# Optimization experiments

Measured on AMD Instinct MI355X. Metric: run time of the kernel, lower is better.

## Reference

```python
import jax, jax.numpy as jnp
import numpy as np

ITERATIONS = 10
EPS = 1e-8
ALPHA = 1.0
BETA = 1.0


def _conv3x3x3(x):
    # all-ones 3x3x3 kernel, padding=1 (SAME), single channel; NCDHW layout
    k = jnp.ones((1, 1, 3, 3, 3), x.dtype)
    return jax.lax.conv_general_dilated(
        x, k, window_strides=(1, 1, 1), padding='SAME',
        dimension_numbers=('NCDHW', 'OIDHW', 'NCDHW'))


def _soft_skeletonize(x):
    x = jax.nn.sigmoid(x)
    skeleton = x
    for _ in range(ITERATIONS):
        eroded = (_conv3x3x3(skeleton) > 0).astype(x.dtype)
        opened = (_conv3x3x3(eroded) > 0).astype(x.dtype)
        skeleton = jnp.clip(skeleton - opened, 0.0, 1.0)
    return skeleton


def _count_components(binary):
    neighbors = _conv3x3x3(binary)
    mask = binary > 0
    cnt = jnp.sum(mask).astype(binary.dtype)
    # torch.mean(neighbors[mask] + eps) == sum((neighbors+eps)*mask)/cnt
    mean_nb = jnp.sum(jnp.where(mask, neighbors + EPS, 0.0)) / jnp.maximum(cnt, 1.0)
    return (cnt / mean_nb)[None]


def setup_inputs() -> dict:
    key = jax.random.key(0)
    k1, k2 = jax.random.split(key)
    pred = jax.random.normal(k1, (2, 1, 192, 192, 192), dtype=jnp.float32)
    target = jax.random.uniform(k2, (2, 1, 192, 192, 192), dtype=jnp.float32)
    return {"pred": pred, "target": target}


def reference(pred, target):
    pred_prob = jax.nn.sigmoid(pred)
    # NOTE: module applies sigmoid again inside _soft_skeletonize (faithful)
    pred_skeleton = _soft_skeletonize(pred_prob)
    target_skeleton = _soft_skeletonize(target)

    intersection = jnp.sum(pred_skeleton * target_skeleton)
    union = jnp.sum(pred_skeleton) + jnp.sum(target_skeleton)
    skeleton_loss = 1.0 - (2.0 * intersection + EPS) / (union + EPS)

    pred_binary = (pred_prob > 0.5).astype(pred.dtype)
    target_binary = target  # .float() no-op
    pred_components = _count_components(pred_binary)
    target_components = _count_components(target_binary)
    connectivity_loss = jnp.mean(jnp.abs(pred_components - target_components))

    return ALPHA * skeleton_loss + BETA * connectivity_loss
```

## Files before the change

### kernel.cpp

```cpp
#include <hip/hip_runtime.h>
#include <math.h>

#define NN 192
#define PLANE (NN * NN)
#define VOL (NN * NN * NN)
#define ZCHUNK 12
#define RP 96
#define NBIN 8
#define EPSF 1e-8f

template <int MODE>
__device__ __forceinline__ float bval(float u) {
  return (MODE == 0) ? ((u > 0.f) ? 1.f : 0.f) : u;
}

struct PlaneR {
  float4 a, b, c, d;
};

__device__ __forceinline__ void loadP(const float* __restrict__ base, int z,
                                      int offA, int offB, int offC, int offD,
                                      int xoff, PlaneR& P) {
  const int zz = min(max(z, 0), NN - 1);
  const float* p = base + (size_t)zz * PLANE;
  P.a = *(const float4*)(p + offA + xoff);
  P.b = *(const float4*)(p + offB + xoff);
  P.c = *(const float4*)(p + offC + xoff);
  P.d = *(const float4*)(p + offD + xoff);
}

template <int MODE>
__device__ __forceinline__ void consume2(const PlaneR& P, float mA, float mD, float mz,
                                         int lane, float4& sY, float4& sZ,
                                         float4& cY, float4& cZ) {
  const float a0 = bval<MODE>(P.a.x), a1 = bval<MODE>(P.a.y), a2 = bval<MODE>(P.a.z), a3 = bval<MODE>(P.a.w);
  const float b0 = bval<MODE>(P.b.x), b1 = bval<MODE>(P.b.y), b2 = bval<MODE>(P.b.z), b3 = bval<MODE>(P.b.w);
  const float c0 = bval<MODE>(P.c.x), c1 = bval<MODE>(P.c.y), c2 = bval<MODE>(P.c.z), c3 = bval<MODE>(P.c.w);
  const float d0 = bval<MODE>(P.d.x), d1 = bval<MODE>(P.d.y), d2 = bval<MODE>(P.d.z), d3 = bval<MODE>(P.d.w);
  const float u0 = b0 + c0, u1 = b1 + c1, u2 = b2 + c2, u3 = b3 + c3;
  const float tY0 = fmaf(a0, mA, u0), tY1 = fmaf(a1, mA, u1), tY2 = fmaf(a2, mA, u2), tY3 = fmaf(a3, mA, u3);
  const float tZ0 = fmaf(d0, mD, u0), tZ1 = fmaf(d1, mD, u1), tZ2 = fmaf(d2, mD, u2), tZ3 = fmaf(d3, mD, u3);
  const float upY = __shfl_up(tY3, 1), dnY = __shfl_down(tY0, 1);
  const float upZ = __shfl_up(tZ3, 1), dnZ = __shfl_down(tZ0, 1);
  const float tlY = (lane == 0) ? 0.f : upY;
  const float trY = (lane >= 47) ? 0.f : dnY;
  const float tlZ = (lane == 0) ? 0.f : upZ;
  const float trZ = (lane >= 47) ? 0.f : dnZ;
  const float pY01 = tY0 + tY1, pY23 = tY2 + tY3;
  const float pZ01 = tZ0 + tZ1, pZ23 = tZ2 + tZ3;
  sY.x = (tlY + pY01) * mz; sY.y = (pY01 + tY2) * mz; sY.z = (tY1 + pY23) * mz; sY.w = (pY23 + trY) * mz;
  sZ.x = (tlZ + pZ01) * mz; sZ.y = (pZ01 + tZ2) * mz; sZ.z = (tZ1 + pZ23) * mz; sZ.w = (pZ23 + trZ) * mz;
  cY.x = b0; cY.y = b1; cY.z = b2; cY.w = b3;
  cZ.x = c0; cZ.y = c1; cZ.z = c2; cZ.w = c3;
}

#define ACC1(C, SP, SC, SN)                                   \
  {                                                           \
    float m = ((C) > 0.f) ? act : 0.f;                        \
    cnt += m;                                                 \
    acc = fmaf(m, ((SP) + (SC)) + (SN), acc);                 \
  }

#define ACCUM8(snY, snZ)                      \
  ACC1(cY.x, spY.x, scY.x, (snY).x)           \
  ACC1(cY.y, spY.y, scY.y, (snY).y)           \
  ACC1(cY.z, spY.z, scY.z, (snY).z)           \
  ACC1(cY.w, spY.w, scY.w, (snY).w)           \
  ACC1(cZ.x, spZ.x, scZ.x, (snZ).x)           \
  ACC1(cZ.y, spZ.y, scZ.y, (snZ).y)           \
  ACC1(cZ.z, spZ.z, scZ.z, (snZ).z)           \
  ACC1(cZ.w, spZ.w, scZ.w, (snZ).w)

#define ROTATE(snY, snZ, cnY, cnZ) \
  spY = scY; scY = snY; spZ = scZ; scZ = snZ; cY = cnY; cZ = cnZ;

#define STEP_R(PSLOT, I)                                                   \
  {                                                                        \
    float4 snY, snZ, cnY, cnZ;                                             \
    consume2<MODE>(PSLOT, mA, mD, 1.f, lane, snY, snZ, cnY, cnZ);          \
    loadP(base, z0 + 4 + (I), offA, offB, offC, offD, xoff, PSLOT);        \
    ACCUM8(snY, snZ);                                                      \
    ROTATE(snY, snZ, cnY, cnZ);                                            \
  }

#define STEP_E(PSLOT, MZ)                                                  \
  {                                                                        \
    float4 snY, snZ, cnY, cnZ;                                             \
    consume2<MODE>(PSLOT, mA, mD, (MZ), lane, snY, snZ, cnY, cnZ);         \
    ACCUM8(snY, snZ);                                                      \
    ROTATE(snY, snZ, cnY, cnZ);                                            \
  }

template <int MODE>
__device__ __forceinline__ void unit2(const float* __restrict__ base, int y0, int z0,
                                      int xoff, float act, int lane,
                                      float& cnt, float& acc) {
  const int offB = y0 * NN;
  const int offA = (y0 > 0 ? y0 - 1 : 0) * NN;
  const int offC = (y0 + 1) * NN;
  const int offD = (y0 + 2 < NN ? y0 + 2 : NN - 1) * NN;
  const float mA = (y0 > 0) ? 1.f : 0.f;
  const float mD = (y0 + 2 < NN) ? 1.f : 0.f;
  const float mzLo = (z0 > 0) ? 1.f : 0.f;
  const float mzHi = (z0 + ZCHUNK < NN) ? 1.f : 0.f;

  PlaneR P0, P1, P2;
  loadP(base, z0 - 1, offA, offB, offC, offD, xoff, P0);
  loadP(base, z0,     offA, offB, offC, offD, xoff, P1);
  loadP(base, z0 + 1, offA, offB, offC, offD, xoff, P2);

  float4 spY, scY, spZ, scZ, cY, cZ, j1, j2;
  consume2<MODE>(P0, mA, mD, mzLo, lane, spY, spZ, j1, j2);
  loadP(base, z0 + 2, offA, offB, offC, offD, xoff, P0);
  consume2<MODE>(P1, mA, mD, 1.f, lane, scY, scZ, cY, cZ);
  loadP(base, z0 + 3, offA, offB, offC, offD, xoff, P1);

#pragma unroll 1
  for (int i = 0; i < 9; i += 3) {
    STEP_R(P2, i + 0);
    STEP_R(P0, i + 1);
    STEP_R(P1, i + 2);
  }
  STEP_E(P2, 1.f);
  STEP_E(P0, 1.f);
  STEP_E(P1, mzHi);
}

__global__ void init_ws(float* __restrict__ ws) {
  if (threadIdx.x < NBIN * 16) ws[threadIdx.x] = 0.f;
}

__global__ __launch_bounds__(64, 4) void skel_main(const float* __restrict__ pred,
                                                   const float* __restrict__ target,
                                                   float* __restrict__ ws) {
  const int b = blockIdx.x;
  const int vol = b & 3;
  const int r = b >> 2;
  const int zc = r / RP;
  const int yp = r % RP;
  const int z0 = zc * ZCHUNK;
  const int y0 = 2 * yp;
  const float* base = (vol < 2 ? pred : target) + (size_t)(vol & 1) * VOL;

  const int lane = threadIdx.x;
  const int xoff = 4 * min(lane, 47);
  const float act = (lane < 48) ? 1.f : 0.f;

  float cnt = 0.f, acc = 0.f;
  if (vol < 2) unit2<0>(base, y0, z0, xoff, act, lane, cnt, acc);
  else         unit2<1>(base, y0, z0, xoff, act, lane, cnt, acc);

#pragma unroll
  for (int o = 32; o > 0; o >>= 1) {
    cnt += __shfl_down(cnt, o);
    acc += __shfl_down(acc, o);
  }
  if (lane == 0) {
    const int off = (vol < 2) ? 0 : 2;
    float* slot = &ws[((r & (NBIN - 1)) << 4) + off];
    atomicAdd(slot + 0, cnt);
    atomicAdd(slot + 1, acc);
  }
}

__global__ void finalize(const float* __restrict__ ws, float* __restrict__ out) {
  if (threadIdx.x == 0 && blockIdx.x == 0) {
    float cp = 0.f, ap = 0.f, ct = 0.f, at = 0.f;
#pragma unroll
    for (int i = 0; i < NBIN; ++i) {
      cp += ws[i * 16 + 0];
      ap += ws[i * 16 + 1];
      ct += ws[i * 16 + 2];
      at += ws[i * 16 + 3];
    }
    float mp = (ap + EPSF * cp) / fmaxf(cp, 1.f);
    float Pc = cp / mp;
    float mt = (at + EPSF * ct) / fmaxf(ct, 1.f);
    float Tc = ct / mt;
    out[0] = fabsf(Pc - Tc);
  }
}

extern "C" void kernel_launch(void* const* d_in, const int* in_sizes, int n_in,
                              void* d_out, int out_size, void* d_ws, size_t ws_size,
                              hipStream_t stream) {
  const float* pred = (const float*)d_in[0];
  const float* target = (const float*)d_in[1];
  float* ws = (float*)d_ws;
  float* out = (float*)d_out;

  init_ws<<<1, 128, 0, stream>>>(ws);
  skel_main<<<dim3(6144), dim3(64), 0, stream>>>(pred, target, ws);
  finalize<<<1, 64, 0, stream>>>(ws, out);
}
```

Measured before the change: 163.2 us.

## Stage 10-row y-slabs through LDS ring buffer with 256-thread blocks

Replaces per-wave direct global loads of 4 rows per z-plane with a 4-slot LDS ring buffer. A 256-thread block cooperatively loads a 10-row slab (8 rows plus halos) per plane, and each of its 4 waves reads its own 4-row window from LDS. This cuts redundant global reads of the y-halo rows, from about 2x down to about 1.25x, and lengthens the z-chunk to 24, which lowers z-halo overhead. Block indexing is remapped so the low bits select the z-chunk, presumably to spread work across XCDs. The cost is a __syncthreads per plane, fewer and larger blocks (768), and an extra block-level reduction through shared memory.

```diff
diff --git a/kernel.cpp b/kernel.cpp
--- a/kernel.cpp
+++ b/kernel.cpp
@@ -3,9 +3,11 @@
 
 #define NN 192
 #define PLANE (NN * NN)
-#define VOL (NN * NN * NN)
-#define ZCHUNK 12
-#define RP 96
+#define VOLSZ (NN * NN * NN)
+#define ZC 24
+#define SLABR 8
+#define NSLAB (NN / SLABR)
+#define SLOTF (10 * NN)
 #define NBIN 8
 #define EPSF 1e-8f
 
@@ -17,17 +19,6 @@
 struct PlaneR {
   float4 a, b, c, d;
 };
-
-__device__ __forceinline__ void loadP(const float* __restrict__ base, int z,
-                                      int offA, int offB, int offC, int offD,
-                                      int xoff, PlaneR& P) {
-  const int zz = min(max(z, 0), NN - 1);
-  const float* p = base + (size_t)zz * PLANE;
-  P.a = *(const float4*)(p + offA + xoff);
-  P.b = *(const float4*)(p + offB + xoff);
-  P.c = *(const float4*)(p + offC + xoff);
-  P.d = *(const float4*)(p + offD + xoff);
-}
 
 template <int MODE>
 __device__ __forceinline__ void consume2(const PlaneR& P, float mA, float mD, float mz,
@@ -71,95 +62,141 @@
   ACC1(cZ.z, spZ.z, scZ.z, (snZ).z)           \
   ACC1(cZ.w, spZ.w, scZ.w, (snZ).w)
 
-#define ROTATE(snY, snZ, cnY, cnZ) \
-  spY = scY; scY = snY; spZ = scZ; scZ = snZ; cY = cnY; cZ = cnZ;
-
-#define STEP_R(PSLOT, I)                                                   \
+__device__ __forceinline__ void ldsReadP(const float* pl, int slotF, int rbaseF, int xoff, PlaneR& P) {
+  const float* p = pl + slotF + rbaseF;
+  P.a = *(const float4*)(p + 0 * NN + xoff);
+  P.b = *(const float4*)(p + 1 * NN + xoff);
+  P.c = *(const float4*)(p + 2 * NN + xoff);
+  P.d = *(const float4*)(p + 3 * NN + xoff);
+}
+
+__device__ __forceinline__ void stageIssue(const float* __restrict__ base, int z, int gRow0,
+                                           int tid, int nQ, float4& g0, float4& g1) {
+  const int zz = min(max(z, 0), NN - 1);
+  const float* gp = base + (size_t)zz * PLANE + gRow0 * NN;
+  g0 = *(const float4*)(gp + 4 * tid);
+  if (tid + 256 < nQ) g1 = *(const float4*)(gp + 4 * (tid + 256));
+}
+
+__device__ __forceinline__ void stageWrite(float* pl, int slotF, int shiftF, int tid, int nQ,
+                                           const float4& g0, const float4& g1) {
+  float* q = pl + slotF + shiftF;
+  *(float4*)(q + 4 * tid) = g0;
+  if (tid + 256 < nQ) *(float4*)(q + 4 * (tid + 256)) = g1;
+}
+
+#define STEPX(RS, WS, DO_A, DO_B, ZLD, G0, G1, MZ)                         \
   {                                                                        \
+    __syncthreads();                                                       \
+    if (DO_A) stageWrite(pl, (WS) * SLOTF, shiftF, tid, nQ, G0, G1);       \
+    if (DO_B) stageIssue(base, (ZLD), gRow0, tid, nQ, G0, G1);             \
+    PlaneR P;                                                              \
+    ldsReadP(pl, (RS) * SLOTF, rbaseF, xoff, P);                           \
     float4 snY, snZ, cnY, cnZ;                                             \
-    consume2<MODE>(PSLOT, mA, mD, 1.f, lane, snY, snZ, cnY, cnZ);          \
-    loadP(base, z0 + 4 + (I), offA, offB, offC, offD, xoff, PSLOT);        \
+    consume2<MODE>(P, mA, mD, (MZ), lane, snY, snZ, cnY, cnZ);             \
     ACCUM8(snY, snZ);                                                      \
-    ROTATE(snY, snZ, cnY, cnZ);                                            \
-  }
-
-#define STEP_E(PSLOT, MZ)                                                  \
-  {                                                                        \
-    float4 snY, snZ, cnY, cnZ;                                             \
-    consume2<MODE>(PSLOT, mA, mD, (MZ), lane, snY, snZ, cnY, cnZ);         \
-    ACCUM8(snY, snZ);                                                      \
-    ROTATE(snY, snZ, cnY, cnZ);                                            \
+    spY = scY; scY = snY; spZ = scZ; scZ = snZ; cY = cnY; cZ = cnZ;        \
   }
 
 template <int MODE>
-__device__ __forceinline__ void unit2(const float* __restrict__ base, int y0, int z0,
-                                      int xoff, float act, int lane,
-                                      float& cnt, float& acc) {
-  const int offB = y0 * NN;
-  const int offA = (y0 > 0 ? y0 - 1 : 0) * NN;
-  const int offC = (y0 + 1) * NN;
-  const int offD = (y0 + 2 < NN ? y0 + 2 : NN - 1) * NN;
-  const float mA = (y0 > 0) ? 1.f : 0.f;
-  const float mD = (y0 + 2 < NN) ? 1.f : 0.f;
+__device__ __forceinline__ void sweep(const float* __restrict__ base, int y0, int z0,
+                                      float* pl, int tid, float& cnt, float& acc) {
+  const int lane = tid & 63;
+  const int w = tid >> 6;
+  const int xoff = 4 * min(lane, 47);
+  const float act = (lane < 48) ? 1.f : 0.f;
+
+  const bool loEdge = (y0 == 0), hiEdge = (y0 + SLABR == NN);
+  const int gRow0 = loEdge ? 0 : y0 - 1;
+  const int nR = 10 - (loEdge ? 1 : 0) - (hiEdge ? 1 : 0);
+  const int nQ = nR * 48;
+  const int shiftF = loEdge ? NN : 0;
+
+  const int rbaseF = (2 * w) * NN;
+  const float mA = (y0 + 2 * w > 0) ? 1.f : 0.f;
+  const float mD = (y0 + 2 * w + 2 < NN) ? 1.f : 0.f;
   const float mzLo = (z0 > 0) ? 1.f : 0.f;
-  const float mzHi = (z0 + ZCHUNK < NN) ? 1.f : 0.f;
-
-  PlaneR P0, P1, P2;
-  loadP(base, z0 - 1, offA, offB, offC, offD, xoff, P0);
-  loadP(base, z0,     offA, offB, offC, offD, xoff, P1);
-  loadP(base, z0 + 1, offA, offB, offC, offD, xoff, P2);
-
-  float4 spY, scY, spZ, scZ, cY, cZ, j1, j2;
-  consume2<MODE>(P0, mA, mD, mzLo, lane, spY, spZ, j1, j2);
-  loadP(base, z0 + 2, offA, offB, offC, offD, xoff, P0);
-  consume2<MODE>(P1, mA, mD, 1.f, lane, scY, scZ, cY, cZ);
-  loadP(base, z0 + 3, offA, offB, offC, offD, xoff, P1);
+  const float mzHi = (z0 + ZC < NN) ? 1.f : 0.f;
+
+  if (loEdge && tid < 48) {
+    const float4 z4 = make_float4(0.f, 0.f, 0.f, 0.f);
+#pragma unroll
+    for (int r = 0; r < 4; ++r) *(float4*)(pl + r * SLOTF + 4 * tid) = z4;
+  }
+  if (hiEdge && tid < 48) {
+    const float4 z4 = make_float4(0.f, 0.f, 0.f, 0.f);
+#pragma unroll
+    for (int r = 0; r < 4; ++r) *(float4*)(pl + r * SLOTF + 9 * NN + 4 * tid) = z4;
+  }
+
+  float4 a0, a1, b0, b1, c0, c1, gP0, gP1, gQ0, gQ1;
+  stageIssue(base, z0 - 1, gRow0, tid, nQ, a0, a1);
+  stageIssue(base, z0,     gRow0, tid, nQ, b0, b1);
+  stageIssue(base, z0 + 1, gRow0, tid, nQ, c0, c1);
+  stageIssue(base, z0 + 2, gRow0, tid, nQ, gP0, gP1);
+  stageIssue(base, z0 + 3, gRow0, tid, nQ, gQ0, gQ1);
+  stageWrite(pl, 0 * SLOTF, shiftF, tid, nQ, a0, a1);
+  stageWrite(pl, 1 * SLOTF, shiftF, tid, nQ, b0, b1);
+  stageWrite(pl, 2 * SLOTF, shiftF, tid, nQ, c0, c1);
+  __syncthreads();
+
+  float4 spY, scY, spZ, scZ, cY, cZ;
+  {
+    PlaneR P; float4 j1, j2;
+    ldsReadP(pl, 0, rbaseF, xoff, P);
+    consume2<MODE>(P, mA, mD, mzLo, lane, spY, spZ, j1, j2);
+    ldsReadP(pl, SLOTF, rbaseF, xoff, P);
+    consume2<MODE>(P, mA, mD, 1.f, lane, scY, scZ, cY, cZ);
+  }
 
 #pragma unroll 1
-  for (int i = 0; i < 9; i += 3) {
-    STEP_R(P2, i + 0);
-    STEP_R(P0, i + 1);
-    STEP_R(P1, i + 2);
-  }
-  STEP_E(P2, 1.f);
-  STEP_E(P0, 1.f);
-  STEP_E(P1, mzHi);
+  for (int j = 0; j < 20; j += 4) {
+    STEPX(2, 3, true, true, z0 + 4 + j + 0, gP0, gP1, 1.f);
+    STEPX(3, 0, true, true, z0 + 4 + j + 1, gQ0, gQ1, 1.f);
+    STEPX(0, 1, true, true, z0 + 4 + j + 2, gP0, gP1, 1.f);
+    STEPX(1, 2, true, true, z0 + 4 + j + 3, gQ0, gQ1, 1.f);
+  }
+  STEPX(2, 3, true, true,  z0 + 24, gP0, gP1, 1.f);
+  STEPX(3, 0, true, false, 0,       gQ0, gQ1, 1.f);
+  STEPX(0, 1, true, false, 0,       gP0, gP1, 1.f);
+  STEPX(1, 2, false, false, 0,      gQ0, gQ1, mzHi);
 }
 
 __global__ void init_ws(float* __restrict__ ws) {
   if (threadIdx.x < NBIN * 16) ws[threadIdx.x] = 0.f;
 }
 
-__global__ __launch_bounds__(64, 4) void skel_main(const float* __restrict__ pred,
-                                                   const float* __restrict__ target,
-                                                   float* __restrict__ ws) {
+__global__ __launch_bounds__(256, 1) void skel_main(const float* __restrict__ pred,
+                                                    const float* __restrict__ target,
+                                                    float* __restrict__ ws) {
+  __shared__ float pl[4 * SLOTF];
   const int b = blockIdx.x;
-  const int vol = b & 3;
-  const int r = b >> 2;
-  const int zc = r / RP;
-  const int yp = r % RP;
-  const int z0 = zc * ZCHUNK;
-  const int y0 = 2 * yp;
-  const float* base = (vol < 2 ? pred : target) + (size_t)(vol & 1) * VOL;
-
-  const int lane = threadIdx.x;
-  const int xoff = 4 * min(lane, 47);
-  const float act = (lane < 48) ? 1.f : 0.f;
+  const int xcd = b & 7;
+  const int s = b >> 3;
+  const int vol = s / NSLAB;
+  const int slab = s % NSLAB;
+  const int z0 = xcd * ZC;
+  const int y0 = slab * SLABR;
+  const float* base = (vol < 2 ? pred : target) + (size_t)(vol & 1) * VOLSZ;
+  const int tid = threadIdx.x;
 
   float cnt = 0.f, acc = 0.f;
-  if (vol < 2) unit2<0>(base, y0, z0, xoff, act, lane, cnt, acc);
-  else         unit2<1>(base, y0, z0, xoff, act, lane, cnt, acc);
+  if (vol < 2) sweep<0>(base, y0, z0, pl, tid, cnt, acc);
+  else         sweep<1>(base, y0, z0, pl, tid, cnt, acc);
 
 #pragma unroll
   for (int o = 32; o > 0; o >>= 1) {
     cnt += __shfl_down(cnt, o);
     acc += __shfl_down(acc, o);
   }
-  if (lane == 0) {
+  __syncthreads();
+  if ((tid & 63) == 0) { pl[tid >> 6] = cnt; pl[4 + (tid >> 6)] = acc; }
+  __syncthreads();
+  if (tid == 0) {
     const int off = (vol < 2) ? 0 : 2;
-    float* slot = &ws[((r & (NBIN - 1)) << 4) + off];
-    atomicAdd(slot + 0, cnt);
-    atomicAdd(slot + 1, acc);
+    float* sp = &ws[((slab & (NBIN - 1)) << 4) + off];
+    atomicAdd(sp + 0, pl[0] + pl[1] + pl[2] + pl[3]);
+    atomicAdd(sp + 1, pl[4] + pl[5] + pl[6] + pl[7]);
   }
 }
 
@@ -190,6 +227,6 @@
   float* out = (float*)d_out;
 
   init_ws<<<1, 128, 0, stream>>>(ws);
-  skel_main<<<dim3(6144), dim3(64), 0, stream>>>(pred, target, ws);
+  skel_main<<<dim3(768), dim3(256), 0, stream>>>(pred, target, ws);
   finalize<<<1, 64, 0, stream>>>(ws, out);
 }
```

Measured after the change: 133.9 us. 1.22x faster.
